# Performance work log

Measured on AMD Instinct MI355X. Metric: run time of the kernel, lower is better.

## Reference

```python
import jax, jax.numpy as jnp
import numpy as np

B = 8192
FULL_DIM = 4096
HEADS = 16
MLP_DIM = 16384
CHUNKS = 4
HEAD_IN = FULL_DIM // HEADS      # 256
HEAD_OUT = MLP_DIM // HEADS      # 1024
CHUNK = HEAD_IN // CHUNKS        # 64


def _chunk_random_perm(rng):
    # PermuteIn(mode='chunk_random'): permute 64-wide chunks across full_dim
    n_chunks = FULL_DIM // CHUNK
    chunk_idx = rng.permutation(n_chunks)
    perm = np.concatenate([np.arange(CHUNK) + i * CHUNK for i in chunk_idx])
    return perm.astype(np.int32)


def setup_inputs() -> dict:
    key = jax.random.key(0)
    k1, k2, k3 = jax.random.split(key, 3)
    rng = np.random.default_rng(0)
    # xavier_uniform with relu gain = sqrt(2) on (in_dim, out_dim) matrices
    gain = np.sqrt(2.0)
    bound_up = gain * np.sqrt(6.0 / (HEAD_IN + HEAD_OUT))
    bound_dn = gain * np.sqrt(6.0 / (HEAD_OUT + HEAD_IN))
    return {
        "x": jax.random.normal(k1, (B, FULL_DIM), dtype=jnp.float32),
        "perm": jnp.asarray(_chunk_random_perm(rng)),
        "w_up": jax.random.uniform(k2, (HEADS, HEAD_IN, HEAD_OUT), jnp.float32, -bound_up, bound_up),
        "b_up": jnp.zeros((MLP_DIM,), jnp.float32),
        "w_down": jax.random.uniform(k3, (HEADS, HEAD_OUT, HEAD_IN), jnp.float32, -bound_dn, bound_dn),
        "b_down": jnp.zeros((FULL_DIM,), jnp.float32),
    }


def reference(x, perm, w_up, b_up, w_down, b_down):
    b = x.shape[0]
    unperm = jnp.argsort(perm)  # inverse permutation (Unpermute)
    # PermuteIn
    h = x[:, perm]
    # up: per-head grouped GEMM + bias
    h = h.reshape(b, HEADS, HEAD_IN)
    h = jnp.einsum('bhd,hdl->bhl', h, w_up).reshape(b, MLP_DIM) + b_up
    # GELU (exact, matching torch nn.GELU default)
    h = jax.nn.gelu(h, approximate=False)
    # down: per-head grouped GEMM + bias
    h = h.reshape(b, HEADS, HEAD_OUT)
    h = jnp.einsum('bhd,hdl->bhl', h, w_down).reshape(b, FULL_DIM) + b_down
    # Unpermute
    return h[:, unperm]
```

## Files before the change

### kernel.cpp

```cpp
#include <hip/hip_runtime.h>
#include <hip/hip_bf16.h>
#include <math.h>

#define HEADS    16
#define HEAD_IN  256
#define HEAD_OUT 1024
#define FULLD    4096
#define BM       128
#define NC       32
#define NCHUNKS  (HEAD_OUT / NC)
#define THREADS  256
#define LDO      268

typedef short  short8 __attribute__((ext_vector_type(8)));
typedef float  f32x4  __attribute__((ext_vector_type(4)));
typedef float  f32x16 __attribute__((ext_vector_type(16)));
typedef unsigned int u32;

#define AS_GLOBAL __attribute__((address_space(1)))
#define AS_LOCAL  __attribute__((address_space(3)))

__device__ __forceinline__ void gload_lds16(const void* g, void* l) {
    __builtin_amdgcn_global_load_lds((const AS_GLOBAL u32*)g, (AS_LOCAL u32*)l, 16, 0, 0);
}

__device__ __forceinline__ ushort f2bf(float f) {
    union { float f; unsigned u; } x; x.f = f;
    unsigned r = x.u + 0x7fffu + ((x.u >> 16) & 1u);
    return (ushort)(r >> 16);
}

__device__ __forceinline__ float fast_gelu(float v) {
    float v2 = v * v;
    float p  = __builtin_fmaf(v2, 0.044715f, 1.0f);
    float a  = v * p * -2.3021254f;
    float e  = __builtin_amdgcn_exp2f(a);
    float r  = __builtin_amdgcn_rcpf(1.0f + e);
    return v * r;
}

__global__ void __launch_bounds__(256) transpose_head(const float* __restrict__ in,
                                                      ushort* __restrict__ out,
                                                      int R, int C) {
    __shared__ __align__(16) ushort tile[64][68];
    int h = blockIdx.z;
    const float* ip = in  + (size_t)h * R * C;
    ushort*      op = out + (size_t)h * R * C;
    int t  = threadIdx.x;
    int cr = t & 15;
    int rr = t >> 4;
    int r0 = blockIdx.x * 64, c0 = blockIdx.y * 64;
    #pragma unroll
    for (int p = 0; p < 4; ++p) {
        int r = rr + p * 16;
        float4 v = *(const float4*)&ip[(size_t)(r0 + r) * C + c0 + cr * 4];
        tile[r][cr*4+0] = f2bf(v.x); tile[r][cr*4+1] = f2bf(v.y);
        tile[r][cr*4+2] = f2bf(v.z); tile[r][cr*4+3] = f2bf(v.w);
    }
    __syncthreads();
    #pragma unroll
    for (int p = 0; p < 4; ++p) {
        int c = rr + p * 16;
        ushort4 v;
        v.x = tile[cr*4+0][c]; v.y = tile[cr*4+1][c];
        v.z = tile[cr*4+2][c]; v.w = tile[cr*4+3][c];
        *(ushort4*)&op[(size_t)(c0 + c) * R + r0 + cr * 4] = v;
    }
}

__global__ void __launch_bounds__(THREADS, 2)
fused_mlp(const float* __restrict__ x, const int* __restrict__ perm,
          const ushort* __restrict__ wupT, const float* __restrict__ bup,
          const ushort* __restrict__ wdnT, const float* __restrict__ bdn,
          float* __restrict__ out) {
    __shared__ __align__(16) char smem[2 * 32768];

    const int t    = threadIdx.x;
    const int wave = t >> 6;
    const int lane = t & 63;
    const int rho  = lane & 31;
    const int h5   = lane >> 5;
    const int h    = blockIdx.y;
    const int m0   = blockIdx.x * BM;

    const ushort* g1b[4];
    const ushort* g2b[4];
    #pragma unroll
    for (int p = 0; p < 4; ++p) {
        int row = p*8 + wave*2 + h5;
        int n   = (row & 0x13) | ((row & 4) << 1) | ((row & 8) >> 1);
        g1b[p] = wupT + (((size_t)h*HEAD_OUT + n) << 8) + (rho ^ (row & 7)) * 8;
        int d  = p*64 + wave*16 + (lane >> 2);
        g2b[p] = wdnT + (((size_t)h*HEAD_IN + d) << 10) + ((lane & 3) ^ (d & 3)) * 8;
    }
    char* l1b = smem + wave*1024;
    char* l2b = smem + 16384 + wave*1024;

    #pragma unroll
    for (int p = 0; p < 4; ++p) {
        gload_lds16(g1b[p], l1b + p*4096);
        gload_lds16(g2b[p], l2b + p*4096);
    }

    short8 xf[16];
    {
        const float* xrow = x + (size_t)(m0 + wave*32 + rho) * FULLD;
        #pragma unroll
        for (int ks = 0; ks < 16; ++ks) {
            int g = perm[h*HEAD_IN + ks*16 + h5*8];
            float4 a = *(const float4*)(xrow + g);
            float4 b = *(const float4*)(xrow + g + 4);
            short8 v;
            v[0]=(short)f2bf(a.x); v[1]=(short)f2bf(a.y);
            v[2]=(short)f2bf(a.z); v[3]=(short)f2bf(a.w);
            v[4]=(short)f2bf(b.x); v[5]=(short)f2bf(b.y);
            v[6]=(short)f2bf(b.z); v[7]=(short)f2bf(b.w);
            xf[ks] = v;
        }
    }

    f32x16 oacc[8];
    #pragma unroll
    for (int i = 0; i < 8; ++i)
        #pragma unroll
        for (int e = 0; e < 16; ++e) oacc[i][e] = 0.f;

    const float* bupb = bup + h*HEAD_OUT + h5*8;
    const int x1 = rho & 7;
    const int x2 = rho & 3;

    __syncthreads();

    for (int ch = 0; ch < NCHUNKS; ++ch) {
        const int buf = (ch & 1) * 32768;

        if (ch + 1 < NCHUNKS) {
            const int nbuf = ((ch + 1) & 1) * 32768;
            const size_t d1 = (size_t)(ch + 1) * (NC * 256);
            const size_t d2 = (size_t)(ch + 1) * NC;
            #pragma unroll
            for (int p = 0; p < 4; ++p) {
                gload_lds16(g1b[p] + d1, l1b + nbuf + p*4096);
                gload_lds16(g2b[p] + d2, l2b + nbuf + p*4096);
            }
        }

        const char* s1 = smem + buf + rho*512;
        f32x16 te, to;
        #pragma unroll
        for (int e = 0; e < 16; ++e) { te[e] = 0.f; to[e] = 0.f; }
        #pragma unroll
        for (int ks = 0; ks < 16; ks += 2) {
            short8 w0 = *(const short8*)(s1 + ((((ks    )*2 + h5) ^ x1) * 16));
            short8 w1 = *(const short8*)(s1 + ((((ks + 1)*2 + h5) ^ x1) * 16));
            te = __builtin_amdgcn_mfma_f32_32x32x16_bf16(w0, xf[ks],     te, 0, 0, 0);
            to = __builtin_amdgcn_mfma_f32_32x32x16_bf16(w1, xf[ks + 1], to, 0, 0, 0);
        }

        short8 a2[2];
        #pragma unroll
        for (int kk = 0; kk < 2; ++kk) {
            f32x4 bA = *(const f32x4*)(bupb + ch*NC + kk*16);
            f32x4 bB = *(const f32x4*)(bupb + ch*NC + kk*16 + 4);
            short8 v;
            #pragma unroll
            for (int e = 0; e < 4; ++e) {
                float u0 = te[kk*8 + e]     + to[kk*8 + e]     + bA[e];
                float u1 = te[kk*8 + 4 + e] + to[kk*8 + 4 + e] + bB[e];
                v[e]     = (short)f2bf(fast_gelu(u0));
                v[4 + e] = (short)f2bf(fast_gelu(u1));
            }
            a2[kk] = v;
        }

        const char* s2 = smem + buf + 16384 + rho*64;
        #pragma unroll
        for (int kk = 0; kk < 2; ++kk) {
            #pragma unroll
            for (int dt = 0; dt < 8; ++dt) {
                short8 b = *(const short8*)(s2 + dt*2048 + (((kk*2 + h5) ^ x2) * 16));
                oacc[dt] = __builtin_amdgcn_mfma_f32_32x32x16_bf16(a2[kk], b, oacc[dt], 0, 0, 0);
            }
        }

        __syncthreads();
    }

    float* sOutF = (float*)smem;
    #pragma unroll
    for (int quar = 0; quar < 4; ++quar) {
        __syncthreads();
        if (wave == quar) {
            #pragma unroll
            for (int dt = 0; dt < 8; ++dt) {
                const float bias = bdn[h*HEAD_IN + dt*32 + rho];
                #pragma unroll
                for (int rg = 0; rg < 16; ++rg) {
                    int row = (rg & 3) + 8*(rg >> 2) + 4*h5;
                    sOutF[row*LDO + dt*32 + rho] = oacc[dt][rg] + bias;
                }
            }
        }
        __syncthreads();
        #pragma unroll
        for (int i = 0; i < 4; ++i) {
            int idx = i*THREADS + t;
            int mr  = idx >> 5;
            int sg  = idx & 31;
            int g   = perm[h*HEAD_IN + sg*8];
            const float* src = sOutF + mr*LDO + sg*8;
            float4 v0 = *(const float4*)src;
            float4 v1 = *(const float4*)(src + 4);
            float* dst = out + (size_t)(m0 + quar*32 + mr)*FULLD + g;
            *(float4*)dst       = v0;
            *(float4*)(dst + 4) = v1;
        }
    }
}

extern "C" void kernel_launch(void* const* d_in, const int* in_sizes, int n_in,
                              void* d_out, int out_size, void* d_ws, size_t ws_size,
                              hipStream_t stream) {
    const float* x    = (const float*)d_in[0];
    const int*   perm = (const int*)d_in[1];
    const float* wup  = (const float*)d_in[2];
    const float* bup  = (const float*)d_in[3];
    const float* wdn  = (const float*)d_in[4];
    const float* bdn  = (const float*)d_in[5];
    float* out = (float*)d_out;

    const int Bt = in_sizes[0] / FULLD;
    const size_t wcount = (size_t)HEADS * HEAD_IN * HEAD_OUT;

    ushort* wupT = (ushort*)d_ws;
    ushort* wdnT = wupT + wcount;

    transpose_head<<<dim3(HEAD_IN/64,  HEAD_OUT/64, HEADS), 256, 0, stream>>>(wup, wupT, HEAD_IN,  HEAD_OUT);
    transpose_head<<<dim3(HEAD_OUT/64, HEAD_IN/64,  HEADS), 256, 0, stream>>>(wdn, wdnT, HEAD_OUT, HEAD_IN);

    dim3 grid(Bt / BM, HEADS, 1);
    fused_mlp<<<grid, THREADS, 0, stream>>>(x, perm, wupT, bup, wdnT, bdn, out);
}
```

Measured before the change: 478.2 us.

## Enlarge block to 256 rows with triple-buffered weight pipeline and XCD-aware head mapping

Doubles the rows per block (8 waves, 512 threads) so each streamed weight chunk is reused across more rows. Switches from a double-buffered LDS ring to a triple-buffered one that waits on vmcnt and a single barrier per chunk. Remaps block indices so each XCD owns two heads for better L2 locality of weights, and raises wave priority around MFMA bursts. In exchange it uses 96KB of LDS and allows fewer resident blocks per CU. The swizzle pattern and the grid mapping are hardcoded for B=8192.

```diff
diff --git a/kernel.cpp b/kernel.cpp
--- a/kernel.cpp
+++ b/kernel.cpp
@@ -6,11 +6,12 @@
 #define HEAD_IN  256
 #define HEAD_OUT 1024
 #define FULLD    4096
-#define BM       128
+#define BM       256
 #define NC       32
 #define NCHUNKS  (HEAD_OUT / NC)
-#define THREADS  256
+#define THREADS  512
 #define LDO      268
+#define BUFSZ    32768
 
 typedef short  short8 __attribute__((ext_vector_type(8)));
 typedef float  f32x4  __attribute__((ext_vector_type(4)));
@@ -73,41 +74,51 @@
           const ushort* __restrict__ wupT, const float* __restrict__ bup,
           const ushort* __restrict__ wdnT, const float* __restrict__ bdn,
           float* __restrict__ out) {
-    __shared__ __align__(16) char smem[2 * 32768];
+    __shared__ __align__(16) char smem[3 * BUFSZ];
 
     const int t    = threadIdx.x;
     const int wave = t >> 6;
     const int lane = t & 63;
     const int rho  = lane & 31;
     const int h5   = lane >> 5;
-    const int h    = blockIdx.y;
-    const int m0   = blockIdx.x * BM;
-
-    const ushort* g1b[4];
-    const ushort* g2b[4];
-    #pragma unroll
-    for (int p = 0; p < 4; ++p) {
-        int row = p*8 + wave*2 + h5;
-        int n   = (row & 0x13) | ((row & 4) << 1) | ((row & 8) >> 1);
-        g1b[p] = wupT + (((size_t)h*HEAD_OUT + n) << 8) + (rho ^ (row & 7)) * 8;
-        int d  = p*64 + wave*16 + (lane >> 2);
-        g2b[p] = wdnT + (((size_t)h*HEAD_IN + d) << 10) + ((lane & 3) ^ (d & 3)) * 8;
-    }
-    char* l1b = smem + wave*1024;
-    char* l2b = smem + 16384 + wave*1024;
-
-    #pragma unroll
-    for (int p = 0; p < 4; ++p) {
-        gload_lds16(g1b[p], l1b + p*4096);
-        gload_lds16(g2b[p], l2b + p*4096);
+
+    const int bflat = blockIdx.x + (blockIdx.y << 5);
+    const int xcd   = bflat & 7;
+    const int bidx  = bflat >> 3;
+    const int h     = xcd * 2 + (bidx >> 5);
+    const int m0    = (bidx & 31) * BM;
+
+    const ushort* g1s[2];
+    const ushort* g2s[2];
+    #pragma unroll
+    for (int a = 0; a < 2; ++a) {
+        int j = a * THREADS + t;
+        int p = j >> 5, s = j & 31;
+        int n = (p & 0x13) | ((p & 4) << 1) | ((p & 8) >> 1);
+        g1s[a] = wupT + (((size_t)h * HEAD_OUT + n) << 8) + (s ^ (p & 7)) * 8;
+        int d = j >> 2, sq = j & 3;
+        g2s[a] = wdnT + (((size_t)h * HEAD_IN + d) << 10) + (sq ^ ((d >> 1) & 3)) * 8;
+    }
+    char* l1d = smem + wave * 1024;
+    char* l2d = smem + 16384 + wave * 1024;
+
+    #pragma unroll
+    for (int a = 0; a < 2; ++a) {
+        gload_lds16(g1s[a], l1d + a * 8192);
+        gload_lds16(g2s[a], l2d + a * 8192);
+    }
+    #pragma unroll
+    for (int a = 0; a < 2; ++a) {
+        gload_lds16(g1s[a] + (size_t)NC * 256, l1d + BUFSZ + a * 8192);
+        gload_lds16(g2s[a] + NC,               l2d + BUFSZ + a * 8192);
     }
 
     short8 xf[16];
     {
-        const float* xrow = x + (size_t)(m0 + wave*32 + rho) * FULLD;
+        const float* xrow = x + (size_t)(m0 + wave * 32 + rho) * FULLD;
         #pragma unroll
         for (int ks = 0; ks < 16; ++ks) {
-            int g = perm[h*HEAD_IN + ks*16 + h5*8];
+            int g = perm[h * HEAD_IN + ks * 16 + h5 * 8];
             float4 a = *(const float4*)(xrow + g);
             float4 b = *(const float4*)(xrow + g + 4);
             short8 v;
@@ -125,43 +136,43 @@
         #pragma unroll
         for (int e = 0; e < 16; ++e) oacc[i][e] = 0.f;
 
-    const float* bupb = bup + h*HEAD_OUT + h5*8;
+    const float* bupb = bup + h * HEAD_OUT + h5 * 8;
     const int x1 = rho & 7;
-    const int x2 = rho & 3;
-
-    __syncthreads();
-
+    const int x2 = (rho >> 1) & 3;
+
+    int cur = 0;
     for (int ch = 0; ch < NCHUNKS; ++ch) {
-        const int buf = (ch & 1) * 32768;
-
-        if (ch + 1 < NCHUNKS) {
-            const int nbuf = ((ch + 1) & 1) * 32768;
-            const size_t d1 = (size_t)(ch + 1) * (NC * 256);
-            const size_t d2 = (size_t)(ch + 1) * NC;
-            #pragma unroll
-            for (int p = 0; p < 4; ++p) {
-                gload_lds16(g1b[p] + d1, l1b + nbuf + p*4096);
-                gload_lds16(g2b[p] + d2, l2b + nbuf + p*4096);
-            }
-        }
-
-        const char* s1 = smem + buf + rho*512;
+        asm volatile("s_waitcnt vmcnt(4)\n\ts_barrier" ::: "memory");
+
+        {
+            int cc = ch + 2 < NCHUNKS ? ch + 2 : NCHUNKS - 1;
+            int pf = cur - BUFSZ; if (pf < 0) pf += 3 * BUFSZ;
+            #pragma unroll
+            for (int a = 0; a < 2; ++a) {
+                gload_lds16(g1s[a] + (size_t)cc * (NC * 256), l1d + pf + a * 8192);
+                gload_lds16(g2s[a] + (size_t)cc * NC,         l2d + pf + a * 8192);
+            }
+        }
+
+        const char* s1 = smem + cur + rho * 512;
         f32x16 te, to;
         #pragma unroll
         for (int e = 0; e < 16; ++e) { te[e] = 0.f; to[e] = 0.f; }
+        __builtin_amdgcn_s_setprio(1);
         #pragma unroll
         for (int ks = 0; ks < 16; ks += 2) {
-            short8 w0 = *(const short8*)(s1 + ((((ks    )*2 + h5) ^ x1) * 16));
-            short8 w1 = *(const short8*)(s1 + ((((ks + 1)*2 + h5) ^ x1) * 16));
+            short8 w0 = *(const short8*)(s1 + ((((ks    ) * 2 + h5) ^ x1) * 16));
+            short8 w1 = *(const short8*)(s1 + ((((ks + 1) * 2 + h5) ^ x1) * 16));
             te = __builtin_amdgcn_mfma_f32_32x32x16_bf16(w0, xf[ks],     te, 0, 0, 0);
             to = __builtin_amdgcn_mfma_f32_32x32x16_bf16(w1, xf[ks + 1], to, 0, 0, 0);
         }
+        __builtin_amdgcn_s_setprio(0);
 
         short8 a2[2];
         #pragma unroll
         for (int kk = 0; kk < 2; ++kk) {
-            f32x4 bA = *(const f32x4*)(bupb + ch*NC + kk*16);
-            f32x4 bB = *(const f32x4*)(bupb + ch*NC + kk*16 + 4);
+            f32x4 bA = *(const f32x4*)(bupb + ch * NC + kk * 16);
+            f32x4 bB = *(const f32x4*)(bupb + ch * NC + kk * 16 + 4);
             short8 v;
             #pragma unroll
             for (int e = 0; e < 4; ++e) {
@@ -173,45 +184,50 @@
             a2[kk] = v;
         }
 
-        const char* s2 = smem + buf + 16384 + rho*64;
+        const char* s2 = smem + cur + 16384 + rho * 64;
+        __builtin_amdgcn_s_setprio(1);
         #pragma unroll
         for (int kk = 0; kk < 2; ++kk) {
             #pragma unroll
             for (int dt = 0; dt < 8; ++dt) {
-                short8 b = *(const short8*)(s2 + dt*2048 + (((kk*2 + h5) ^ x2) * 16));
+                short8 b = *(const short8*)(s2 + dt * 2048 + (((kk * 2 + h5) ^ x2) * 16));
                 oacc[dt] = __builtin_amdgcn_mfma_f32_32x32x16_bf16(a2[kk], b, oacc[dt], 0, 0, 0);
             }
         }
-
-        __syncthreads();
-    }
+        __builtin_amdgcn_s_setprio(0);
+
+        cur += BUFSZ; if (cur == 3 * BUFSZ) cur = 0;
+    }
+
+    __syncthreads();
 
     float* sOutF = (float*)smem;
     #pragma unroll
-    for (int quar = 0; quar < 4; ++quar) {
-        __syncthreads();
-        if (wave == quar) {
+    for (int ro = 0; ro < 4; ++ro) {
+        if (ro) __syncthreads();
+        if ((wave >> 1) == ro) {
+            const int wl = wave & 1;
             #pragma unroll
             for (int dt = 0; dt < 8; ++dt) {
-                const float bias = bdn[h*HEAD_IN + dt*32 + rho];
+                const float bias = bdn[h * HEAD_IN + dt * 32 + rho];
                 #pragma unroll
                 for (int rg = 0; rg < 16; ++rg) {
-                    int row = (rg & 3) + 8*(rg >> 2) + 4*h5;
-                    sOutF[row*LDO + dt*32 + rho] = oacc[dt][rg] + bias;
+                    int row = wl * 32 + (rg & 3) + 8 * (rg >> 2) + 4 * h5;
+                    sOutF[row * LDO + dt * 32 + rho] = oacc[dt][rg] + bias;
                 }
             }
         }
         __syncthreads();
         #pragma unroll
         for (int i = 0; i < 4; ++i) {
-            int idx = i*THREADS + t;
+            int idx = i * THREADS + t;
             int mr  = idx >> 5;
             int sg  = idx & 31;
-            int g   = perm[h*HEAD_IN + sg*8];
-            const float* src = sOutF + mr*LDO + sg*8;
+            int g   = perm[h * HEAD_IN + sg * 8];
+            const float* src = sOutF + mr * LDO + sg * 8;
             float4 v0 = *(const float4*)src;
             float4 v1 = *(const float4*)(src + 4);
-            float* dst = out + (size_t)(m0 + quar*32 + mr)*FULLD + g;
+            float* dst = out + (size_t)(m0 + ro * 64 + mr) * FULLD + g;
             *(float4*)dst       = v0;
             *(float4*)(dst + 4) = v1;
         }
```

After: 472.6 us. Within noise of the previous version (-1.2%).
